# Kernel tuning notes

Hardware: AMD Instinct MI355X
Metric: run time of the kernel (lower is better)

Reference implementation:

```python
import jax, jax.numpy as jnp
import numpy as np

B, S, E, A, H = 512, 128, 640, 129, 2048   # batch, seq=num_actions-1, embed_dim, num_actions, hidden
NHEADS, HD = 10, E // 10
K = int(A * 0.5)  # num_winners = 64
NEG = -1e9


def _ln(x, g, b):
    m = x.mean(-1, keepdims=True)
    v = ((x - m) ** 2).mean(-1, keepdims=True)
    return (x - m) / jnp.sqrt(v + 1e-5) * g + b


def setup_inputs() -> dict:
    key = jax.random.key(0)
    ks = jax.random.split(key, 20)
    u = lambda k, shape: jax.random.uniform(k, shape, minval=-0.03, maxval=0.03, dtype=jnp.float32)
    return {
        "hist_state": jax.random.normal(ks[0], (B, S, E), jnp.float32),
        "last_action": jax.nn.softmax(jax.random.normal(ks[1], (B, A), jnp.float32), axis=-1),
        "embed_w": u(ks[2], (E, E)), "embed_b": u(ks[3], (E,)),
        "in_proj_w": jax.random.normal(ks[4], (3 * E, E), jnp.float32) * np.sqrt(2.0 / E).astype(np.float32),
        "in_proj_b": jnp.zeros((3 * E,), jnp.float32),
        "out_proj_w": u(ks[5], (E, E)), "out_proj_b": jnp.zeros((E,), jnp.float32),
        "lnorm_g": jnp.ones((E,), jnp.float32), "lnorm_b": jnp.zeros((E,), jnp.float32),
        "fc1_w": u(ks[6], (H, E * S + A)), "fc1_b": u(ks[7], (H,)),
        "fc2_w": u(ks[8], (H, H)), "fc2_b": u(ks[9], (H,)),
        "ln1_g": jnp.ones((H,), jnp.float32), "ln1_b": jnp.zeros((H,), jnp.float32),
        "fc3_w": u(ks[10], (H // 2, H)), "fc3_b": u(ks[11], (H // 2,)),
        "fc4_w": u(ks[12], (H // 4, H // 2)), "fc4_b": u(ks[13], (H // 4,)),
        "fc5_w": u(ks[14], (A, H // 4)), "fc5_b": u(ks[15], (A,)),
        "fc6_w": u(ks[16], (A, 2 * A)), "fc6_b": u(ks[17], (A,)),
    }


def reference(hist_state, last_action, embed_w, embed_b, in_proj_w, in_proj_b,
              out_proj_w, out_proj_b, lnorm_g, lnorm_b, fc1_w, fc1_b, fc2_w, fc2_b,
              ln1_g, ln1_b, fc3_w, fc3_b, fc4_w, fc4_b, fc5_w, fc5_b, fc6_w, fc6_b):
    # embed + self-attention (MultiheadAttention, batch_first)
    h = hist_state @ embed_w.T + embed_b                       # [B,S,E]
    qkv = h @ in_proj_w.T + in_proj_b                          # [B,S,3E]
    q, k, v = jnp.split(qkv, 3, axis=-1)
    split = lambda t: t.reshape(B, S, NHEADS, HD).transpose(0, 2, 1, 3)  # [B,h,S,d]
    q, k, v = split(q) * (HD ** -0.5), split(k), split(v)
    attn = jax.nn.softmax(jnp.einsum('bhqd,bhkd->bhqk', q, k), axis=-1)
    ctx = jnp.einsum('bhqk,bhkd->bhqd', attn, v).transpose(0, 2, 1, 3).reshape(B, S, E)
    attn_out = ctx @ out_proj_w.T + out_proj_b
    x = _ln(attn_out + h, lnorm_g, lnorm_b)
    # flatten + MLP with residual
    x = jnp.concatenate([x.reshape(B, -1), last_action], axis=1)  # [B, E*S+A]
    x = jax.nn.relu(x @ fc1_w.T + fc1_b)
    temp = x
    x = jax.nn.relu(x @ fc2_w.T + fc2_b) + temp
    x = _ln(x, ln1_g, ln1_b)
    x = jax.nn.relu(x @ fc3_w.T + fc3_b)
    x = jax.nn.relu(x @ fc4_w.T + fc4_b)
    x = x @ fc5_w.T + fc5_b
    x = jnp.concatenate([x, last_action], axis=1)
    final_scores = x @ fc6_w.T + fc6_b                          # [B,A]
    # per-row top-K winners mask + masked softmax (trade mask is always all-True)
    _, win_idx = jax.lax.top_k(final_scores, K)                 # [B,K]
    losers_mask = jnp.ones_like(final_scores).at[jnp.arange(B)[:, None], win_idx].set(0.0) * NEG
    return jax.nn.softmax(final_scores + losers_mask, axis=1)
```

## Files before the change

kernel.cpp:

```cpp
#include <hip/hip_runtime.h>


#define BB   512
#define SS   128
#define EE   640
#define AA   129
#define HH   2048
#define NH   10
#define HD   64

#define WS_QKV      0LL
#define WS_W2HI     0LL
#define WS_W2LO     8388608LL
#define WS_W3HI     16777216LL
#define WS_W3LO     20971520LL
#define WS_W4HI     25165824LL
#define WS_W4LO     26214400LL
#define WS_HHI      503316480LL
#define WS_HLO      587202560LL
#define WS_XHI      503316480LL
#define WS_XLO      587202560LL
#define WS_EMBHI    671088640LL
#define WS_EMBLO    671907840LL
#define WS_INPHI    672727040LL
#define WS_INPLO    675184640LL
#define WS_OUTHI    677642240LL
#define WS_OUTLO    678461440LL
#define WS_C1       671088640LL
#define WS_C2       675282944LL
#define WS_C3       679477248LL
#define WS_C4       681574400LL
#define WS_X1HI     682622976LL
#define WS_X1LO     684720128LL
#define WS_X2HI     686817280LL
#define WS_X2LO     688914432LL
#define WS_X3HI     691011584LL
#define WS_X3LO     692060160LL
#define WS_X4F      693108736LL
#define WS_ZERO_LEN 11534336LL

typedef __bf16 bf16x8 __attribute__((ext_vector_type(8)));
typedef float  f32x4  __attribute__((ext_vector_type(4)));
typedef unsigned short us8 __attribute__((ext_vector_type(8)));
typedef unsigned short us4 __attribute__((ext_vector_type(4)));

__device__ __forceinline__ unsigned int bf16_rne(float x) {
    unsigned int u = __float_as_uint(x);
    return (u + 0x7fffu + ((u >> 16) & 1u)) >> 16;
}
__device__ __forceinline__ void split2(float x, unsigned short& h, unsigned short& l) {
    const unsigned int hb = bf16_rne(x);
    const float hf = __uint_as_float(hb << 16);
    const unsigned int lb = bf16_rne(x - hf);
    h = (unsigned short)hb; l = (unsigned short)lb;
}
__device__ __forceinline__ void split2fast(float x, unsigned short& h, unsigned short& l) {
    const unsigned int u  = __float_as_uint(x);
    const unsigned int hb = u & 0xffff0000u;
    const float lf = x - __uint_as_float(hb);
    h = (unsigned short)(u >> 16);
    l = (unsigned short)(__float_as_uint(lf) >> 16);
}
__device__ __forceinline__ float bf2f(unsigned short v) {
    return __uint_as_float((unsigned int)v << 16);
}

__device__ __forceinline__ void gload16(const unsigned short* g, unsigned short* l) {
    __builtin_amdgcn_global_load_lds(
        (__attribute__((address_space(1))) unsigned int*)g,
        (__attribute__((address_space(3))) unsigned int*)l, 16, 0, 0);
}

__device__ __forceinline__ void stage_otf(const float* src, int align4,
                                          unsigned short* dhi, unsigned short* dlo) {
    float f[8];
    if (align4) {
        const float4 v0 = *reinterpret_cast<const float4*>(src);
        const float4 v1 = *reinterpret_cast<const float4*>(src + 4);
        f[0] = v0.x; f[1] = v0.y; f[2] = v0.z; f[3] = v0.w;
        f[4] = v1.x; f[5] = v1.y; f[6] = v1.z; f[7] = v1.w;
    } else {
#pragma unroll
        for (int j = 0; j < 8; ++j) f[j] = src[j];
    }
    us8 h, l;
#pragma unroll
    for (int j = 0; j < 8; ++j) {
        unsigned short hh, ll; split2fast(f[j], hh, ll);
        h[j] = hh; l[j] = ll;
    }
    *reinterpret_cast<us8*>(dhi) = h;
    *reinterpret_cast<us8*>(dlo) = l;
}

struct MGemmP {
    const unsigned short *Ahi, *Alo, *Bhi, *Blo;
    const float *Af32, *Bf32;
    float* C;
    const float* bias; const float* resid;
    const unsigned short *Rhi, *Rlo;
    unsigned short *Chi, *Clo;
    long long lda, ldb, ldc, ldr;
    int kChunk; int act; int aAlign4, bAlign4;
};

template <bool ATOMIC, bool AOTF, bool BOTF>
__global__ __launch_bounds__(256, 2)
void gemm_mfma(MGemmP p) {
    __shared__ __align__(16) unsigned short sAhi[4096];
    __shared__ __align__(16) unsigned short sAlo[4096];
    __shared__ __align__(16) unsigned short sBhi[4096];
    __shared__ __align__(16) unsigned short sBlo[4096];
    const int tid = threadIdx.x;
    const int lane = tid & 63, wave = tid >> 6;
    const int n0 = blockIdx.x * 128, m0 = blockIdx.y * 128;
    const long long kS = (long long)blockIdx.z * p.kChunk;
    const long long kE = kS + p.kChunk;
    const int wr = (wave >> 1) * 64, wc = (wave & 1) * 64;

    int aoff[4], boff[4];
#pragma unroll
    for (int i = 0; i < 4; ++i) {
        const int ks = lane >> 4;
        const int ar = wr + i * 16 + (lane & 15);
        aoff[i] = (ar * 4 + (ks ^ ((ar >> 1) & 3))) * 8;
        const int br = wc + i * 16 + (lane & 15);
        boff[i] = (br * 4 + (ks ^ ((br >> 1) & 3))) * 8;
    }

    long long gA[2], gB[2];
    int ldsU[2], ldsP[2];
#pragma unroll
    for (int c = 0; c < 2; ++c) {
        const int ch = c * 256 + tid;
        const int r  = ch >> 2;
        const int s  = (ch & 3) ^ ((r >> 1) & 3);
        gA[c] = (long long)(m0 + r) * p.lda + s * 8;
        gB[c] = (long long)(n0 + r) * p.ldb + s * 8;
        ldsU[c] = (c * 256 + wave * 64) * 8;
        ldsP[c] = ch * 8;
    }

    f32x4 acc[4][4];
    const f32x4 zero = {0.f, 0.f, 0.f, 0.f};
#pragma unroll
    for (int i = 0; i < 4; ++i)
#pragma unroll
        for (int j = 0; j < 4; ++j) acc[i][j] = zero;

    for (long long kt = kS; kt < kE; kt += 32) {
#pragma unroll
        for (int c = 0; c < 2; ++c) {
            if (AOTF) {
                stage_otf(p.Af32 + gA[c] + kt, p.aAlign4, &sAhi[ldsP[c]], &sAlo[ldsP[c]]);
            } else {
                gload16(p.Ahi + gA[c] + kt, &sAhi[ldsU[c]]);
                gload16(p.Alo + gA[c] + kt, &sAlo[ldsU[c]]);
            }
            if (BOTF) {
                stage_otf(p.Bf32 + gB[c] + kt, p.bAlign4, &sBhi[ldsP[c]], &sBlo[ldsP[c]]);
            } else {
                gload16(p.Bhi + gB[c] + kt, &sBhi[ldsU[c]]);
                gload16(p.Blo + gB[c] + kt, &sBlo[ldsU[c]]);
            }
        }
        __syncthreads();
        bf16x8 ah[4], al[4], bh[4], bl[4];
#pragma unroll
        for (int i = 0; i < 4; ++i) {
            ah[i] = *(const bf16x8*)&sAhi[aoff[i]];
            al[i] = *(const bf16x8*)&sAlo[aoff[i]];
            bh[i] = *(const bf16x8*)&sBhi[boff[i]];
            bl[i] = *(const bf16x8*)&sBlo[boff[i]];
        }
#pragma unroll
        for (int mi = 0; mi < 4; ++mi)
#pragma unroll
            for (int ni = 0; ni < 4; ++ni) {
                acc[mi][ni] = __builtin_amdgcn_mfma_f32_16x16x32_bf16(ah[mi], bh[ni], acc[mi][ni], 0, 0, 0);
                acc[mi][ni] = __builtin_amdgcn_mfma_f32_16x16x32_bf16(ah[mi], bl[ni], acc[mi][ni], 0, 0, 0);
                acc[mi][ni] = __builtin_amdgcn_mfma_f32_16x16x32_bf16(al[mi], bh[ni], acc[mi][ni], 0, 0, 0);
            }
        __syncthreads();
    }

    const int rb = (lane >> 4) * 4, ci = lane & 15;
#pragma unroll
    for (int mi = 0; mi < 4; ++mi)
#pragma unroll
        for (int r = 0; r < 4; ++r) {
            const long long row = (long long)(m0 + wr + mi * 16 + rb + r);
#pragma unroll
            for (int ni = 0; ni < 4; ++ni) {
                const int col = n0 + wc + ni * 16 + ci;
                float v = acc[mi][ni][r];
                if (ATOMIC) {
                    unsafeAtomicAdd(&p.C[row * p.ldc + col], v);
                } else {
                    if (p.bias)  v += p.bias[col];
                    if (p.resid) v += p.resid[row * p.ldr + col];
                    if (p.Rhi) {
                        const long long ri = row * p.ldr + col;
                        v += bf2f(p.Rhi[ri]) + bf2f(p.Rlo[ri]);
                    }
                    if (p.act)   v = fmaxf(v, 0.f);
                    if (p.C)     p.C[row * p.ldc + col] = v;
                    if (p.Chi) {
                        unsigned short h, l; split2(v, h, l);
                        p.Chi[row * p.ldc + col] = h;
                        p.Clo[row * p.ldc + col] = l;
                    }
                }
            }
        }
}

struct GemmP {
    const float* A; const float* B; float* C;
    const float* bias; const float* resid;
    int lda, ldb, ldc, ldr;
    int kStart, kEnd, kChunk, kOffA;
    int act;
};

template <bool ATOMIC>
__global__ __launch_bounds__(256)
void gemm128(GemmP p) {
    __shared__ float As[16 * 128];
    __shared__ float Bs[16 * 128];
    const int tid = threadIdx.x;
    const int m0 = blockIdx.x * 128;
    const int n0 = blockIdx.y * 128;
    int kS = p.kStart + (int)blockIdx.z * p.kChunk;
    int kE = kS + p.kChunk; if (kE > p.kEnd) kE = p.kEnd;
    const int tx = tid & 15, ty = tid >> 4;

    float acc[8][8];
#pragma unroll
    for (int i = 0; i < 8; ++i)
#pragma unroll
        for (int j = 0; j < 8; ++j) acc[i][j] = 0.f;

    const bool a4 = ((p.lda & 3) == 0);
    const bool b4 = ((p.ldb & 3) == 0);

    for (int kt = kS; kt < kE; kt += 16) {
#pragma unroll
        for (int it = 0; it < 2; ++it) {
            const int slot = tid + it * 256;
            const int row = slot >> 2;
            const int kq  = (slot & 3) << 2;
            const int k   = kt + kq;
            {
                const float* ap = p.A + (long long)(m0 + row) * p.lda + (k - p.kOffA);
                float4 v;
                if (a4 && (k + 4 <= kE)) {
                    v = *reinterpret_cast<const float4*>(ap);
                } else {
                    v.x = (k + 0 < kE) ? ap[0] : 0.f;
                    v.y = (k + 1 < kE) ? ap[1] : 0.f;
                    v.z = (k + 2 < kE) ? ap[2] : 0.f;
                    v.w = (k + 3 < kE) ? ap[3] : 0.f;
                }
                As[(kq + 0) * 128 + row] = v.x;
                As[(kq + 1) * 128 + row] = v.y;
                As[(kq + 2) * 128 + row] = v.z;
                As[(kq + 3) * 128 + row] = v.w;
            }
            {
                const float* bp = p.B + (long long)(n0 + row) * p.ldb + k;
                float4 v;
                if (b4 && (k + 4 <= kE)) {
                    v = *reinterpret_cast<const float4*>(bp);
                } else {
                    v.x = (k + 0 < kE) ? bp[0] : 0.f;
                    v.y = (k + 1 < kE) ? bp[1] : 0.f;
                    v.z = (k + 2 < kE) ? bp[2] : 0.f;
                    v.w = (k + 3 < kE) ? bp[3] : 0.f;
                }
                Bs[(kq + 0) * 128 + row] = v.x;
                Bs[(kq + 1) * 128 + row] = v.y;
                Bs[(kq + 2) * 128 + row] = v.z;
                Bs[(kq + 3) * 128 + row] = v.w;
            }
        }
        __syncthreads();
#pragma unroll
        for (int kk = 0; kk < 16; ++kk) {
            float a[8], b[8];
            *reinterpret_cast<float4*>(&a[0]) = *reinterpret_cast<const float4*>(&As[kk * 128 + ty * 8]);
            *reinterpret_cast<float4*>(&a[4]) = *reinterpret_cast<const float4*>(&As[kk * 128 + ty * 8 + 4]);
            *reinterpret_cast<float4*>(&b[0]) = *reinterpret_cast<const float4*>(&Bs[kk * 128 + tx * 8]);
            *reinterpret_cast<float4*>(&b[4]) = *reinterpret_cast<const float4*>(&Bs[kk * 128 + tx * 8 + 4]);
#pragma unroll
            for (int i = 0; i < 8; ++i)
#pragma unroll
                for (int j = 0; j < 8; ++j) acc[i][j] += a[i] * b[j];
        }
        __syncthreads();
    }

#pragma unroll
    for (int i = 0; i < 8; ++i) {
        const int row = m0 + ty * 8 + i;
        const long long cb = (long long)row * p.ldc + n0 + tx * 8;
        if (ATOMIC) {
#pragma unroll
            for (int j = 0; j < 8; ++j) unsafeAtomicAdd(&p.C[cb + j], acc[i][j]);
        } else {
            const long long rb = (long long)row * p.ldr + n0 + tx * 8;
#pragma unroll
            for (int j = 0; j < 8; ++j) {
                float v = acc[i][j];
                if (p.bias)  v += p.bias[n0 + tx * 8 + j];
                if (p.resid) v += p.resid[rb + j];
                if (p.act)   v = fmaxf(v, 0.f);
                p.C[cb + j] = v;
            }
        }
    }
}

__global__ __launch_bounds__(256)
void split_kernel(const float* __restrict__ in, unsigned short* __restrict__ hi,
                  unsigned short* __restrict__ lo, long long n4) {
    const long long stride = (long long)gridDim.x * 256;
    for (long long i = (long long)blockIdx.x * 256 + threadIdx.x; i < n4; i += stride) {
        const float4 v = reinterpret_cast<const float4*>(in)[i];
        unsigned short h0, h1, h2, h3, l0, l1, l2, l3;
        split2(v.x, h0, l0); split2(v.y, h1, l1);
        split2(v.z, h2, l2); split2(v.w, h3, l3);
        us4 hv = {h0, h1, h2, h3};
        us4 lv = {l0, l1, l2, l3};
        reinterpret_cast<us4*>(hi)[i] = hv;
        reinterpret_cast<us4*>(lo)[i] = lv;
    }
}

__global__ __launch_bounds__(256)
void bias_act_split_kernel(const float* __restrict__ c, const float* __restrict__ bias,
                           unsigned short* __restrict__ hi,
                           unsigned short* __restrict__ lo, int mask) {
    const int idx = blockIdx.x * 256 + threadIdx.x;
    const float v = fmaxf(c[idx] + bias[idx & mask], 0.f);
    unsigned short h, l; split2(v, h, l);
    hi[idx] = h; lo[idx] = l;
}

__global__ __launch_bounds__(256)
void bias_relu_kernel(const float* c, const float* bias, float* out, int mask) {
    const int idx = blockIdx.x * 256 + threadIdx.x;
    out[idx] = fmaxf(c[idx] + bias[idx & mask], 0.f);
}

__global__ __launch_bounds__(256)
void attn_kernel(float* qkv) {
    __shared__ float qs[128 * 65];
    __shared__ float ks[128 * 65];
    __shared__ float sc[128 * 129];
    const int tid = threadIdx.x;
    const int b = blockIdx.x / NH, h = blockIdx.x % NH;
    const long long base = (long long)b * SS * (3 * EE) + h * HD;

    for (int idx = tid; idx < 128 * 64; idx += 256) {
        const int s = idx >> 6, d = idx & 63;
        qs[s * 65 + d] = qkv[base + (long long)s * 1920 + d] * 0.125f;
        ks[s * 65 + d] = qkv[base + 640 + (long long)s * 1920 + d];
    }
    __syncthreads();

    {
        const int tx = tid & 15, ty = tid >> 4;
        const int i0 = ty * 8, j0 = tx * 8;
        float acc[8][8];
#pragma unroll
        for (int i = 0; i < 8; ++i)
#pragma unroll
            for (int j = 0; j < 8; ++j) acc[i][j] = 0.f;
#pragma unroll 4
        for (int d = 0; d < 64; ++d) {
            float qa[8], kb[8];
#pragma unroll
            for (int i = 0; i < 8; ++i) qa[i] = qs[(i0 + i) * 65 + d];
#pragma unroll
            for (int j = 0; j < 8; ++j) kb[j] = ks[(j0 + j) * 65 + d];
#pragma unroll
            for (int i = 0; i < 8; ++i)
#pragma unroll
                for (int j = 0; j < 8; ++j) acc[i][j] += qa[i] * kb[j];
        }
#pragma unroll
        for (int i = 0; i < 8; ++i)
#pragma unroll
            for (int j = 0; j < 8; ++j) sc[(i0 + i) * 129 + (j0 + j)] = acc[i][j];
    }
    __syncthreads();

    if (tid < 128) {
        const int r = tid;
        float m = -3.402823466e38f;
        for (int j = 0; j < 128; ++j) m = fmaxf(m, sc[r * 129 + j]);
        float sum = 0.f;
        for (int j = 0; j < 128; ++j) {
            const float e = expf(sc[r * 129 + j] - m);
            sc[r * 129 + j] = e; sum += e;
        }
        const float inv = 1.f / sum;
        for (int j = 0; j < 128; ++j) sc[r * 129 + j] *= inv;
    }
    __syncthreads();

    for (int idx = tid; idx < 128 * 64; idx += 256) {
        const int s = idx >> 6, d = idx & 63;
        qs[s * 65 + d] = qkv[base + 1280 + (long long)s * 1920 + d];
    }
    __syncthreads();

    {
        const int cx = tid & 7, cy = tid >> 3;
        const int i0 = cy * 4, d0 = cx * 8;
        float acc[4][8];
#pragma unroll
        for (int i = 0; i < 4; ++i)
#pragma unroll
            for (int j = 0; j < 8; ++j) acc[i][j] = 0.f;
#pragma unroll 4
        for (int j = 0; j < 128; ++j) {
            float aa[4], vv[8];
#pragma unroll
            for (int i = 0; i < 4; ++i) aa[i] = sc[(i0 + i) * 129 + j];
#pragma unroll
            for (int t = 0; t < 8; ++t) vv[t] = qs[j * 65 + d0 + t];
#pragma unroll
            for (int i = 0; i < 4; ++i)
#pragma unroll
                for (int t = 0; t < 8; ++t) acc[i][t] += aa[i] * vv[t];
        }
#pragma unroll
        for (int i = 0; i < 4; ++i)
#pragma unroll
            for (int t = 0; t < 8; ++t)
                qkv[base + (long long)(i0 + i) * 1920 + d0 + t] = acc[i][t];
    }
}

__global__ __launch_bounds__(256)
void ln640_split_kernel(const float* __restrict__ in, unsigned short* __restrict__ oh,
                        unsigned short* __restrict__ ol,
                        const float* __restrict__ g, const float* __restrict__ bb) {
    const int wave = threadIdx.x >> 6, lane = threadIdx.x & 63;
    const long long row = (long long)blockIdx.x * 4 + wave;
    const float* x = in + row * 1920;
    float v[10]; float s = 0.f;
#pragma unroll
    for (int i = 0; i < 10; ++i) { v[i] = x[lane + i * 64]; s += v[i]; }
#pragma unroll
    for (int o = 32; o; o >>= 1) s += __shfl_xor(s, o);
    const float mean = s * (1.f / 640.f);
    float vs = 0.f;
#pragma unroll
    for (int i = 0; i < 10; ++i) { const float d = v[i] - mean; vs += d * d; }
#pragma unroll
    for (int o = 32; o; o >>= 1) vs += __shfl_xor(vs, o);
    const float rstd = 1.f / sqrtf(vs * (1.f / 640.f) + 1e-5f);
#pragma unroll
    for (int i = 0; i < 10; ++i) {
        const int c = lane + i * 64;
        const float y = (v[i] - mean) * rstd * g[c] + bb[c];
        unsigned short h, l; split2(y, h, l);
        oh[row * 640 + c] = h; ol[row * 640 + c] = l;
    }
}

__global__ __launch_bounds__(256)
void ln2048_split_kernel(const float* __restrict__ c2, const float* __restrict__ b2,
                         const unsigned short* __restrict__ x1h,
                         const unsigned short* __restrict__ x1l,
                         const float* __restrict__ g, const float* __restrict__ bb,
                         unsigned short* __restrict__ oh, unsigned short* __restrict__ ol) {
    const int wave = threadIdx.x >> 6, lane = threadIdx.x & 63;
    const long long row = (long long)blockIdx.x * 4 + wave;
    float v[32]; float s = 0.f;
#pragma unroll
    for (int i = 0; i < 32; ++i) {
        const int c = lane + i * 64;
        const long long ix = row * 2048 + c;
        const float x1v = bf2f(x1h[ix]) + bf2f(x1l[ix]);
        const float t = fmaxf(c2[ix] + b2[c], 0.f) + x1v;
        v[i] = t; s += t;
    }
#pragma unroll
    for (int o = 32; o; o >>= 1) s += __shfl_xor(s, o);
    const float mean = s * (1.f / 2048.f);
    float vs = 0.f;
#pragma unroll
    for (int i = 0; i < 32; ++i) { const float d = v[i] - mean; vs += d * d; }
#pragma unroll
    for (int o = 32; o; o >>= 1) vs += __shfl_xor(vs, o);
    const float rstd = 1.f / sqrtf(vs * (1.f / 2048.f) + 1e-5f);
#pragma unroll
    for (int i = 0; i < 32; ++i) {
        const int c = lane + i * 64;
        const float y = (v[i] - mean) * rstd * g[c] + bb[c];
        unsigned short h, l; split2(y, h, l);
        oh[row * 2048 + c] = h; ol[row * 2048 + c] = l;
    }
}

__global__ __launch_bounds__(256)
void head_kernel(const float* x4, const float* la,
                 const float* w5, const float* b5,
                 const float* w6, const float* b6, float* out) {
    __shared__ float xs[512];
    __shared__ float ys[258];
    __shared__ float scs[132];
    __shared__ int   win[132];
    __shared__ float red[2];
    const int b = blockIdx.x, tid = threadIdx.x;
    const int wave = tid >> 6, lane = tid & 63;

    xs[tid]       = x4[b * 512 + tid];
    xs[tid + 256] = x4[b * 512 + tid + 256];
    if (tid < 129) ys[129 + tid] = la[b * 129 + tid];
    __syncthreads();

    for (int n = wave; n < 129; n += 4) {
        float acc = 0.f;
        for (int k = lane; k < 512; k += 64) acc += w5[n * 512 + k] * xs[k];
#pragma unroll
        for (int o = 32; o; o >>= 1) acc += __shfl_xor(acc, o);
        if (lane == 0) ys[n] = acc + b5[n];
    }
    __syncthreads();

    for (int n = wave; n < 129; n += 4) {
        float acc = 0.f;
        for (int k = lane; k < 258; k += 64) acc += w6[n * 258 + k] * ys[k];
#pragma unroll
        for (int o = 32; o; o >>= 1) acc += __shfl_xor(acc, o);
        if (lane == 0) scs[n] = acc + b6[n];
    }
    __syncthreads();

    if (tid < 129) {
        const float x = scs[tid];
        int cnt = 0;
        for (int j = 0; j < 129; ++j) {
            const float sj = scs[j];
            cnt += (sj > x) || (sj == x && j < tid);
        }
        win[tid] = (cnt < 64) ? 1 : 0;
    }
    __syncthreads();

    if (tid < 64) {
        float m = -3.402823466e38f;
        for (int j = tid; j < 129; j += 64) if (win[j]) m = fmaxf(m, scs[j]);
#pragma unroll
        for (int o = 32; o; o >>= 1) m = fmaxf(m, __shfl_xor(m, o));
        if (tid == 0) red[0] = m;
    }
    __syncthreads();
    if (tid < 129) scs[tid] = win[tid] ? expf(scs[tid] - red[0]) : 0.f;
    __syncthreads();
    if (tid < 64) {
        float s = 0.f;
        for (int j = tid; j < 129; j += 64) s += scs[j];
#pragma unroll
        for (int o = 32; o; o >>= 1) s += __shfl_xor(s, o);
        if (tid == 0) red[1] = s;
    }
    __syncthreads();
    if (tid < 129) out[b * 129 + tid] = scs[tid] / red[1];
}

extern "C" void kernel_launch(void* const* d_in, const int* in_sizes, int n_in,
                              void* d_out, int out_size, void* d_ws, size_t ws_size,
                              hipStream_t stream) {
    (void)in_sizes; (void)n_in; (void)out_size; (void)ws_size;
    const float* hist  = (const float*)d_in[0];
    const float* la    = (const float*)d_in[1];
    const float* emb_w = (const float*)d_in[2];
    const float* emb_b = (const float*)d_in[3];
    const float* inp_w = (const float*)d_in[4];
    const float* inp_b = (const float*)d_in[5];
    const float* out_w = (const float*)d_in[6];
    const float* out_b = (const float*)d_in[7];
    const float* ln_g  = (const float*)d_in[8];
    const float* ln_b  = (const float*)d_in[9];
    const float* w1    = (const float*)d_in[10];
    const float* b1    = (const float*)d_in[11];
    const float* w2    = (const float*)d_in[12];
    const float* b2    = (const float*)d_in[13];
    const float* l1g   = (const float*)d_in[14];
    const float* l1b   = (const float*)d_in[15];
    const float* w3    = (const float*)d_in[16];
    const float* b3    = (const float*)d_in[17];
    const float* w4    = (const float*)d_in[18];
    const float* b4    = (const float*)d_in[19];
    const float* w5    = (const float*)d_in[20];
    const float* b5    = (const float*)d_in[21];
    const float* w6    = (const float*)d_in[22];
    const float* b6    = (const float*)d_in[23];

    char* ws = (char*)d_ws;
    float* qkv = (float*)(ws + WS_QKV);
    float* c1  = (float*)(ws + WS_C1);
    float* c2  = (float*)(ws + WS_C2);
    float* c3  = (float*)(ws + WS_C3);
    float* c4  = (float*)(ws + WS_C4);
    float* x4f = (float*)(ws + WS_X4F);
    typedef unsigned short u16;
    u16* hhi  = (u16*)(ws + WS_HHI);  u16* hlo  = (u16*)(ws + WS_HLO);
    u16* xhi  = (u16*)(ws + WS_XHI);  u16* xlo  = (u16*)(ws + WS_XLO);
    u16* embhi= (u16*)(ws + WS_EMBHI);u16* emblo= (u16*)(ws + WS_EMBLO);
    u16* inphi= (u16*)(ws + WS_INPHI);u16* inplo= (u16*)(ws + WS_INPLO);
    u16* outhi= (u16*)(ws + WS_OUTHI);u16* outlo= (u16*)(ws + WS_OUTLO);
    u16* w2hi = (u16*)(ws + WS_W2HI); u16* w2lo = (u16*)(ws + WS_W2LO);
    u16* w3hi = (u16*)(ws + WS_W3HI); u16* w3lo = (u16*)(ws + WS_W3LO);
    u16* w4hi = (u16*)(ws + WS_W4HI); u16* w4lo = (u16*)(ws + WS_W4LO);
    u16* x1hi = (u16*)(ws + WS_X1HI); u16* x1lo = (u16*)(ws + WS_X1LO);
    u16* x2hi = (u16*)(ws + WS_X2HI); u16* x2lo = (u16*)(ws + WS_X2LO);
    u16* x3hi = (u16*)(ws + WS_X3HI); u16* x3lo = (u16*)(ws + WS_X3LO);

    split_kernel<<<dim3(400),  256, 0, stream>>>(emb_w, embhi, emblo, 102400LL);
    split_kernel<<<dim3(1200), 256, 0, stream>>>(inp_w, inphi, inplo, 307200LL);
    split_kernel<<<dim3(400),  256, 0, stream>>>(out_w, outhi, outlo, 102400LL);

    {
        MGemmP p{}; p.Af32 = hist; p.Bhi = embhi; p.Blo = emblo;
        p.Chi = hhi; p.Clo = hlo; p.bias = emb_b;
        p.lda = 640; p.ldb = 640; p.ldc = 640;
        p.kChunk = 640; p.aAlign4 = 1;
        gemm_mfma<false, true, false><<<dim3(5, 512, 1), 256, 0, stream>>>(p);
    }
    {
        MGemmP p{}; p.Ahi = hhi; p.Alo = hlo; p.Bhi = inphi; p.Blo = inplo;
        p.C = qkv; p.bias = inp_b;
        p.lda = 640; p.ldb = 640; p.ldc = 1920;
        p.kChunk = 640;
        gemm_mfma<false, false, false><<<dim3(15, 512, 1), 256, 0, stream>>>(p);
    }
    attn_kernel<<<dim3(BB * NH), 256, 0, stream>>>(qkv);
    {
        MGemmP p{}; p.Af32 = qkv; p.Bhi = outhi; p.Blo = outlo;
        p.C = qkv + 640; p.bias = out_b;
        p.Rhi = hhi; p.Rlo = hlo; p.ldr = 640;
        p.lda = 1920; p.ldb = 640; p.ldc = 1920;
        p.kChunk = 640; p.aAlign4 = 1;
        gemm_mfma<false, true, false><<<dim3(5, 512, 1), 256, 0, stream>>>(p);
    }
    ln640_split_kernel<<<dim3(16384), 256, 0, stream>>>(qkv + 640, xhi, xlo, ln_g, ln_b);
    hipMemsetAsync(ws + WS_C1, 0, (size_t)WS_ZERO_LEN, stream);
    split_kernel<<<dim3(2048), 256, 0, stream>>>(w2, w2hi, w2lo, 1048576LL);
    split_kernel<<<dim3(2048), 256, 0, stream>>>(w3, w3hi, w3lo, 524288LL);
    split_kernel<<<dim3(512),  256, 0, stream>>>(w4, w4hi, w4lo, 131072LL);
    {
        MGemmP p{}; p.Ahi = xhi; p.Alo = xlo; p.Bf32 = w1;
        p.C = c1;
        p.lda = 81920; p.ldb = 82049; p.ldc = 2048;
        p.kChunk = 5120; p.bAlign4 = 0;
        gemm_mfma<true, false, true><<<dim3(16, 4, 16), 256, 0, stream>>>(p);
    }
    {
        GemmP p{la, w1, c1, nullptr, nullptr, 129, 82049, 2048, 0, 81920, 82049, 129, 81920, 0};
        gemm128<true><<<dim3(4, 16, 1), 256, 0, stream>>>(p);
    }
    bias_act_split_kernel<<<dim3(4096), 256, 0, stream>>>(c1, b1, x1hi, x1lo, 2047);
    {
        MGemmP p{}; p.Ahi = x1hi; p.Alo = x1lo; p.Bhi = w2hi; p.Blo = w2lo;
        p.C = c2;
        p.lda = 2048; p.ldb = 2048; p.ldc = 2048;
        p.kChunk = 512;
        gemm_mfma<true, false, false><<<dim3(16, 4, 4), 256, 0, stream>>>(p);
    }
    ln2048_split_kernel<<<dim3(128), 256, 0, stream>>>(c2, b2, x1hi, x1lo, l1g, l1b, x2hi, x2lo);
    {
        MGemmP p{}; p.Ahi = x2hi; p.Alo = x2lo; p.Bhi = w3hi; p.Blo = w3lo;
        p.C = c3;
        p.lda = 2048; p.ldb = 2048; p.ldc = 1024;
        p.kChunk = 256;
        gemm_mfma<true, false, false><<<dim3(8, 4, 8), 256, 0, stream>>>(p);
    }
    bias_act_split_kernel<<<dim3(2048), 256, 0, stream>>>(c3, b3, x3hi, x3lo, 1023);
    {
        MGemmP p{}; p.Ahi = x3hi; p.Alo = x3lo; p.Bhi = w4hi; p.Blo = w4lo;
        p.C = c4;
        p.lda = 1024; p.ldb = 1024; p.ldc = 512;
        p.kChunk = 128;
        gemm_mfma<true, false, false><<<dim3(4, 4, 8), 256, 0, stream>>>(p);
    }
    bias_relu_kernel<<<dim3(1024), 256, 0, stream>>>(c4, b4, x4f, 511);
    head_kernel<<<dim3(512), 256, 0, stream>>>(x4f, la, w5, b5, w6, b6, (float*)d_out);
}
```

Before: 3.928 ms.

## Double-buffer LDS tiles in split-bf16 MFMA GEMM to overlap loads with compute

Turns the GEMM main loop into a two-stage software pipeline. Shared-memory tiles get two buffers, and the global loads for the next K-tile (direct-to-LDS loads, or fp32 register loads for the on-the-fly split path) are issued before the MFMAs on the current tile. The hi/lo split writes then land in the other buffer, so one barrier per iteration remains instead of two. This doubles LDS use to 64KB per block, which may limit the two-blocks-per-CU occupancy, and adds register pressure from the staged fp32 values. The unaligned path also switches to memcpy-based vector loads.

```diff
diff --git a/kernel.cpp b/kernel.cpp
--- a/kernel.cpp
+++ b/kernel.cpp
@@ -71,18 +71,22 @@
         (__attribute__((address_space(3))) unsigned int*)l, 16, 0, 0);
 }
 
-__device__ __forceinline__ void stage_otf(const float* src, int align4,
-                                          unsigned short* dhi, unsigned short* dlo) {
-    float f[8];
+__device__ __forceinline__ void loadf8(const float* src, int align4, float* f) {
     if (align4) {
         const float4 v0 = *reinterpret_cast<const float4*>(src);
         const float4 v1 = *reinterpret_cast<const float4*>(src + 4);
         f[0] = v0.x; f[1] = v0.y; f[2] = v0.z; f[3] = v0.w;
         f[4] = v1.x; f[5] = v1.y; f[6] = v1.z; f[7] = v1.w;
     } else {
-#pragma unroll
-        for (int j = 0; j < 8; ++j) f[j] = src[j];
-    }
+        float4 v0, v1;
+        __builtin_memcpy(&v0, src, 16);
+        __builtin_memcpy(&v1, src + 4, 16);
+        f[0] = v0.x; f[1] = v0.y; f[2] = v0.z; f[3] = v0.w;
+        f[4] = v1.x; f[5] = v1.y; f[6] = v1.z; f[7] = v1.w;
+    }
+}
+__device__ __forceinline__ void splitwrite(const float* f,
+                                           unsigned short* dhi, unsigned short* dlo) {
     us8 h, l;
 #pragma unroll
     for (int j = 0; j < 8; ++j) {
@@ -107,10 +111,10 @@
 template <bool ATOMIC, bool AOTF, bool BOTF>
 __global__ __launch_bounds__(256, 2)
 void gemm_mfma(MGemmP p) {
-    __shared__ __align__(16) unsigned short sAhi[4096];
-    __shared__ __align__(16) unsigned short sAlo[4096];
-    __shared__ __align__(16) unsigned short sBhi[4096];
-    __shared__ __align__(16) unsigned short sBlo[4096];
+    __shared__ __align__(16) unsigned short sAhi[2][4096];
+    __shared__ __align__(16) unsigned short sAlo[2][4096];
+    __shared__ __align__(16) unsigned short sBhi[2][4096];
+    __shared__ __align__(16) unsigned short sBlo[2][4096];
     const int tid = threadIdx.x;
     const int lane = tid & 63, wave = tid >> 6;
     const int n0 = blockIdx.x * 128, m0 = blockIdx.y * 128;
@@ -148,30 +152,16 @@
 #pragma unroll
         for (int j = 0; j < 4; ++j) acc[i][j] = zero;
 
-    for (long long kt = kS; kt < kE; kt += 32) {
-#pragma unroll
-        for (int c = 0; c < 2; ++c) {
-            if (AOTF) {
-                stage_otf(p.Af32 + gA[c] + kt, p.aAlign4, &sAhi[ldsP[c]], &sAlo[ldsP[c]]);
-            } else {
-                gload16(p.Ahi + gA[c] + kt, &sAhi[ldsU[c]]);
-                gload16(p.Alo + gA[c] + kt, &sAlo[ldsU[c]]);
-            }
-            if (BOTF) {
-                stage_otf(p.Bf32 + gB[c] + kt, p.bAlign4, &sBhi[ldsP[c]], &sBlo[ldsP[c]]);
-            } else {
-                gload16(p.Bhi + gB[c] + kt, &sBhi[ldsU[c]]);
-                gload16(p.Blo + gB[c] + kt, &sBlo[ldsU[c]]);
-            }
-        }
-        __syncthreads();
+    float aregs[2][8], bregs[2][8];
+
+    auto computeTile = [&](int buf) {
         bf16x8 ah[4], al[4], bh[4], bl[4];
 #pragma unroll
         for (int i = 0; i < 4; ++i) {
-            ah[i] = *(const bf16x8*)&sAhi[aoff[i]];
-            al[i] = *(const bf16x8*)&sAlo[aoff[i]];
-            bh[i] = *(const bf16x8*)&sBhi[boff[i]];
-            bl[i] = *(const bf16x8*)&sBlo[boff[i]];
+            ah[i] = *(const bf16x8*)&sAhi[buf][aoff[i]];
+            al[i] = *(const bf16x8*)&sAlo[buf][aoff[i]];
+            bh[i] = *(const bf16x8*)&sBhi[buf][boff[i]];
+            bl[i] = *(const bf16x8*)&sBlo[buf][boff[i]];
         }
 #pragma unroll
         for (int mi = 0; mi < 4; ++mi)
@@ -181,8 +171,59 @@
                 acc[mi][ni] = __builtin_amdgcn_mfma_f32_16x16x32_bf16(ah[mi], bl[ni], acc[mi][ni], 0, 0, 0);
                 acc[mi][ni] = __builtin_amdgcn_mfma_f32_16x16x32_bf16(al[mi], bh[ni], acc[mi][ni], 0, 0, 0);
             }
+    };
+
+#pragma unroll
+    for (int c = 0; c < 2; ++c) {
+        if (AOTF) {
+            loadf8(p.Af32 + gA[c] + kS, p.aAlign4, aregs[c]);
+        } else {
+            gload16(p.Ahi + gA[c] + kS, &sAhi[0][ldsU[c]]);
+            gload16(p.Alo + gA[c] + kS, &sAlo[0][ldsU[c]]);
+        }
+        if (BOTF) {
+            loadf8(p.Bf32 + gB[c] + kS, p.bAlign4, bregs[c]);
+        } else {
+            gload16(p.Bhi + gB[c] + kS, &sBhi[0][ldsU[c]]);
+            gload16(p.Blo + gB[c] + kS, &sBlo[0][ldsU[c]]);
+        }
+    }
+#pragma unroll
+    for (int c = 0; c < 2; ++c) {
+        if (AOTF) splitwrite(aregs[c], &sAhi[0][ldsP[c]], &sAlo[0][ldsP[c]]);
+        if (BOTF) splitwrite(bregs[c], &sBhi[0][ldsP[c]], &sBlo[0][ldsP[c]]);
+    }
+    __syncthreads();
+
+    int cur = 0;
+    for (long long kt = kS; kt + 32 < kE; kt += 32) {
+        const int nxt = cur ^ 1;
+        const long long kn = kt + 32;
+#pragma unroll
+        for (int c = 0; c < 2; ++c) {
+            if (AOTF) {
+                loadf8(p.Af32 + gA[c] + kn, p.aAlign4, aregs[c]);
+            } else {
+                gload16(p.Ahi + gA[c] + kn, &sAhi[nxt][ldsU[c]]);
+                gload16(p.Alo + gA[c] + kn, &sAlo[nxt][ldsU[c]]);
+            }
+            if (BOTF) {
+                loadf8(p.Bf32 + gB[c] + kn, p.bAlign4, bregs[c]);
+            } else {
+                gload16(p.Bhi + gB[c] + kn, &sBhi[nxt][ldsU[c]]);
+                gload16(p.Blo + gB[c] + kn, &sBlo[nxt][ldsU[c]]);
+            }
+        }
+        computeTile(cur);
+#pragma unroll
+        for (int c = 0; c < 2; ++c) {
+            if (AOTF) splitwrite(aregs[c], &sAhi[nxt][ldsP[c]], &sAlo[nxt][ldsP[c]]);
+            if (BOTF) splitwrite(bregs[c], &sBhi[nxt][ldsP[c]], &sBlo[nxt][ldsP[c]]);
+        }
         __syncthreads();
-    }
+        cur = nxt;
+    }
+    computeTile(cur);
 
     const int rb = (lane >> 4) * 4, ci = lane & 15;
 #pragma unroll
```

New measurement: 4.045 ms. 3.0% more time.
